# Performance work log

Measured on AMD Instinct MI355X. Metric: run time of the kernel, lower is better.

## Reference

```python
import jax, jax.numpy as jnp
import numpy as np

K_V = 0.5
G_OFF = 0.001
G_ON = 0.005
N_IN = 4096
N_OUT = 4096
BATCH = 8192


def setup_inputs() -> dict:
    key = jax.random.key(0)
    k1, k2, k3 = jax.random.split(key, 3)
    x = jax.random.normal(k1, (BATCH, N_IN), dtype=jnp.float32)
    # RandomNormal(stddev=1/sqrt(neurons_in)) initializer
    w = jax.random.normal(k2, (N_IN, N_OUT), dtype=jnp.float32) / np.sqrt(N_IN)
    # bias initialized to 0 in the module; use small noise so it is non-degenerate
    b = jax.random.normal(k3, (N_OUT,), dtype=jnp.float32) * 0.01
    return {"x": x, "w": w, "b": b}


def reference(x, w, b):
    # combine_weights: fold bias as an extra input row, x gets a ones column
    weights = jnp.concatenate([w, b[None, :]], axis=0)            # (n_in+1, n_out)
    ones = jnp.ones((x.shape[0], 1), dtype=x.dtype)
    voltages = K_V * jnp.concatenate([x, ones], axis=1)           # (B, n_in+1)

    # weights_to_conductances, 'lowest' mapping rule (differential pair)
    max_weight = jnp.max(jnp.abs(weights))
    k_cond = (G_ON - G_OFF) / max_weight
    g_eff = k_cond * weights
    g_pos = G_OFF + jnp.maximum(g_eff, 0.0)                       # even columns
    g_neg = G_OFF - jnp.minimum(g_eff, 0.0)                       # odd columns
    # interleave pos/neg -> (n_in+1, 2*n_out)
    conductances = jnp.stack([g_pos, g_neg], axis=-1).reshape(weights.shape[0], -1)

    # crossbar currents: scaled GEMM
    currents = voltages @ conductances                            # (B, 2*n_out)

    # differential current subtraction + rescale back to weight domain
    total_currents = currents[:, 0::2] - currents[:, 1::2]        # (B, n_out)
    y_disturbed = total_currents / (K_V * k_cond)
    return y_disturbed
```

## Files before the change

### kernel.cpp

```cpp
#include <hip/hip_runtime.h>
#include <cstdint>

typedef unsigned short u16;
typedef __attribute__((ext_vector_type(8))) __bf16 bf16x8;
typedef __attribute__((ext_vector_type(4))) float f32x4;

#define M_DIM 8192
#define N_DIM 4096
#define K_DIM 4096

#define CVT_X_BLOCKS 16384
#define CVT_W_BLOCKS 4096

__device__ __forceinline__ u16 f2bf(float f) {
    union { float f; uint32_t u; } v; v.f = f;
    uint32_t u = v.u;
    u += 0x7FFFu + ((u >> 16) & 1u);
    return (u16)(u >> 16);
}

__global__ __launch_bounds__(256) void cvt_kernel(const float* __restrict__ x,
                                                  const float* __restrict__ w,
                                                  u16* __restrict__ xb,
                                                  u16* __restrict__ wt) {
    const int t = threadIdx.x;
    if (blockIdx.x < CVT_X_BLOCKS) {
        size_t i = ((size_t)blockIdx.x * 256 + t) * 8;
        const float4* p = (const float4*)(x + i);
        float4 v0 = p[0], v1 = p[1];
        uint32_t o0 = (uint32_t)f2bf(v0.x) | ((uint32_t)f2bf(v0.y) << 16);
        uint32_t o1 = (uint32_t)f2bf(v0.z) | ((uint32_t)f2bf(v0.w) << 16);
        uint32_t o2 = (uint32_t)f2bf(v1.x) | ((uint32_t)f2bf(v1.y) << 16);
        uint32_t o3 = (uint32_t)f2bf(v1.z) | ((uint32_t)f2bf(v1.w) << 16);
        uint4 o; o.x = o0; o.y = o1; o.z = o2; o.w = o3;
        *(uint4*)(xb + i) = o;
    } else {
        __shared__ u16 lds[64 * 68];
        const int bid = blockIdx.x - CVT_X_BLOCKS;
        const int k0 = (bid & 63) * 64;
        const int n0 = (bid >> 6) * 64;
#pragma unroll
        for (int i = 0; i < 4; ++i) {
            int idx = i * 256 + t;
            int r = idx >> 4;
            int c4 = (idx & 15) * 4;
            float4 v = *(const float4*)&w[(size_t)(k0 + r) * N_DIM + n0 + c4];
            uint2 o;
            o.x = (uint32_t)f2bf(v.x) | ((uint32_t)f2bf(v.y) << 16);
            o.y = (uint32_t)f2bf(v.z) | ((uint32_t)f2bf(v.w) << 16);
            *(uint2*)&lds[r * 68 + c4] = o;
        }
        __syncthreads();
#pragma unroll
        for (int i = 0; i < 4; ++i) {
            int idx = i * 256 + t;
            int rn  = idx >> 4;
            int ck  = (idx & 15) * 4;
            uint2 o;
            o.x = (uint32_t)lds[(ck + 0) * 68 + rn] | ((uint32_t)lds[(ck + 1) * 68 + rn] << 16);
            o.y = (uint32_t)lds[(ck + 2) * 68 + rn] | ((uint32_t)lds[(ck + 3) * 68 + rn] << 16);
            *(uint2*)&wt[(size_t)(n0 + rn) * K_DIM + k0 + ck] = o;
        }
    }
}

typedef const uint32_t __attribute__((address_space(1)))* gp_t;
typedef uint32_t __attribute__((address_space(3)))* lp_t;

#define BK 64
#define NTILES (K_DIM / BK)
#define TN_TILES (N_DIM / 256)
#define NWG ((M_DIM / 256) * TN_TILES)

__global__ __launch_bounds__(512, 2) void gemm_kernel(const u16* __restrict__ A,
                                                      const u16* __restrict__ Bt,
                                                      const float* __restrict__ bias,
                                                      float* __restrict__ C) {
    __shared__ u16 As[2][2][256][32];
    __shared__ u16 Bs[2][2][256][32];

    const int t    = threadIdx.x;
    const int lane = t & 63;
    const int l16  = lane & 15;
    const int quad = lane >> 4;
    const int wave = t >> 6;
    const int wr   = wave >> 2;
    const int wc   = wave & 3;

    const int bid = blockIdx.x;
    const int wg  = (bid & 7) * (NWG >> 3) + (bid >> 3);
    const int bm  = (wg / TN_TILES) * 256;
    const int bn  = (wg % TN_TILES) * 256;

    const int rC0 = t >> 2;
    const int rC1 = rC0 + 128;
    const int kcS = ((t & 3) ^ ((rC0 >> 1) & 3)) * 8;
    const u16* a0 = A  + (size_t)(bm + rC0) * K_DIM + kcS;
    const u16* a1 = A  + (size_t)(bm + rC1) * K_DIM + kcS;
    const u16* b0 = Bt + (size_t)(bn + rC0) * K_DIM + kcS;
    const u16* b1 = Bt + (size_t)(bn + rC1) * K_DIM + kcS;

    const int sw8 = (quad ^ ((l16 >> 1) & 3)) * 8;

    f32x4 acc[8][4] = {};
    bf16x8 af[4], bf[4];

#define STAGE_A(buf, kh, kk) do {                                                                   \
        __builtin_amdgcn_global_load_lds((gp_t)(a0 + (kk) + (kh) * 32), (lp_t)&As[buf][kh][rC0][(t & 3) * 8], 16, 0, 0); \
        __builtin_amdgcn_global_load_lds((gp_t)(a1 + (kk) + (kh) * 32), (lp_t)&As[buf][kh][rC1][(t & 3) * 8], 16, 0, 0); \
    } while (0)
#define STAGE_B(buf, kh, kk) do {                                                                   \
        __builtin_amdgcn_global_load_lds((gp_t)(b0 + (kk) + (kh) * 32), (lp_t)&Bs[buf][kh][rC0][(t & 3) * 8], 16, 0, 0); \
        __builtin_amdgcn_global_load_lds((gp_t)(b1 + (kk) + (kh) * 32), (lp_t)&Bs[buf][kh][rC1][(t & 3) * 8], 16, 0, 0); \
    } while (0)
#define LDA(buf, kh, mbase)                                                                \
    _Pragma("unroll")                                                                      \
    for (int i = 0; i < 4; ++i)                                                            \
        af[i] = *(const bf16x8*)&As[buf][kh][wr * 128 + ((mbase) + i) * 16 + l16][sw8]
#define LDB(buf, kh)                                                                       \
    _Pragma("unroll")                                                                      \
    for (int j = 0; j < 4; ++j)                                                            \
        bf[j] = *(const bf16x8*)&Bs[buf][kh][wc * 64 + j * 16 + l16][sw8]
#define MFMA16(mbase)                                                                      \
    __builtin_amdgcn_s_setprio(1);                                                         \
    _Pragma("unroll")                                                                      \
    for (int i = 0; i < 4; ++i)                                                            \
        _Pragma("unroll")                                                                  \
        for (int j = 0; j < 4; ++j)                                                        \
            acc[(mbase) + i][j] =                                                          \
                __builtin_amdgcn_mfma_f32_16x16x32_bf16(af[i], bf[j], acc[(mbase) + i][j], 0, 0, 0); \
    __builtin_amdgcn_s_setprio(0)
#define FENCE() asm volatile("" ::: "memory")

    STAGE_A(0, 0, 0); STAGE_B(0, 0, 0);
    STAGE_A(0, 1, 0); STAGE_B(0, 1, 0);
    asm volatile("s_waitcnt vmcnt(4)" ::: "memory");
    __builtin_amdgcn_s_barrier();
    FENCE();

#pragma unroll 2
    for (int tt = 0; tt < NTILES; ++tt) {
        const int nb = tt & 1;
        const int pb = nb ^ 1;
        const int kn = (tt + 1 < NTILES) ? (tt + 1) * BK : 0;

        STAGE_A(pb, 0, kn);
        LDB(nb, 0);
        LDA(nb, 0, 0);
        MFMA16(0);
        STAGE_B(pb, 0, kn);
        LDA(nb, 0, 4);
        MFMA16(4);

        asm volatile("s_waitcnt vmcnt(4)" ::: "memory");
        __builtin_amdgcn_s_barrier();
        FENCE();

        STAGE_A(pb, 1, kn);
        LDB(nb, 1);
        LDA(nb, 1, 0);
        MFMA16(0);
        STAGE_B(pb, 1, kn);
        LDA(nb, 1, 4);
        MFMA16(4);

        asm volatile("s_waitcnt vmcnt(4)" ::: "memory");
        __builtin_amdgcn_s_barrier();
        FENCE();
    }

#pragma unroll
    for (int j = 0; j < 4; ++j) {
        const int col = bn + wc * 64 + j * 16 + l16;
        const float bv = bias[col];
#pragma unroll
        for (int i = 0; i < 8; ++i) {
            const int row = bm + wr * 128 + i * 16 + quad * 4;
#pragma unroll
            for (int r = 0; r < 4; ++r)
                C[(size_t)(row + r) * N_DIM + col] = acc[i][j][r] + bv;
        }
    }
#undef STAGE_A
#undef STAGE_B
#undef LDA
#undef LDB
#undef MFMA16
#undef FENCE
}

extern "C" void kernel_launch(void* const* d_in, const int* in_sizes, int n_in,
                              void* d_out, int out_size, void* d_ws, size_t ws_size,
                              hipStream_t stream) {
    const float* x = (const float*)d_in[0];
    const float* w = (const float*)d_in[1];
    const float* b = (const float*)d_in[2];
    float* out = (float*)d_out;

    u16* xb = (u16*)d_ws;
    u16* wt = xb + (size_t)M_DIM * K_DIM;

    cvt_kernel<<<CVT_X_BLOCKS + CVT_W_BLOCKS, 256, 0, stream>>>(x, w, xb, wt);
    gemm_kernel<<<dim3(NWG), 512, 0, stream>>>(xb, wt, b, out);
}
```

Measured before the change: 538.4 us.

## Transpose W in registers without LDS and simplify GEMM to BK=32 double buffering

The weight conversion kernel now transposes an 8x4 block per thread in registers and writes 16-byte rows of the transposed bf16 matrix, with no LDS staging and no block barrier. This halves the number of conversion blocks. The GEMM main loop drops the split-half K schedule, which interleaved staging, LDS reads and MFMAs. It now uses a plain K-tile of 32: issue the next tile's async loads, wait, barrier, load all fragments, run 32 MFMAs, then barrier again. This doubles the barriers per unit of K and removes the fine-grained overlap of loads with MFMA, so latency hiding may suffer.

New measurement: 553.8 us. +2.9%, slower.

```diff
diff --git a/kernel.cpp b/kernel.cpp
--- a/kernel.cpp
+++ b/kernel.cpp
@@ -10,7 +10,7 @@
 #define K_DIM 4096
 
 #define CVT_X_BLOCKS 16384
-#define CVT_W_BLOCKS 4096
+#define CVT_W_BLOCKS 2048
 
 __device__ __forceinline__ u16 f2bf(float f) {
     union { float f; uint32_t u; } v; v.f = f;
@@ -35,31 +35,30 @@
         uint4 o; o.x = o0; o.y = o1; o.z = o2; o.w = o3;
         *(uint4*)(xb + i) = o;
     } else {
-        __shared__ u16 lds[64 * 68];
         const int bid = blockIdx.x - CVT_X_BLOCKS;
         const int k0 = (bid & 63) * 64;
-        const int n0 = (bid >> 6) * 64;
+        const int n0 = (bid >> 6) * 128;
+        const int wv = t >> 6, l = t & 63;
+        const int a  = l & 7;
+        const int g  = l >> 3;
+        const int kk = k0 + a * 8;
+        const int nn = n0 + wv * 32 + g * 4;
+
+        uint32_t b[8][4];
+#pragma unroll
+        for (int j = 0; j < 8; ++j) {
+            float4 v = *(const float4*)&w[(size_t)(kk + j) * N_DIM + nn];
+            b[j][0] = f2bf(v.x); b[j][1] = f2bf(v.y);
+            b[j][2] = f2bf(v.z); b[j][3] = f2bf(v.w);
+        }
 #pragma unroll
         for (int i = 0; i < 4; ++i) {
-            int idx = i * 256 + t;
-            int r = idx >> 4;
-            int c4 = (idx & 15) * 4;
-            float4 v = *(const float4*)&w[(size_t)(k0 + r) * N_DIM + n0 + c4];
-            uint2 o;
-            o.x = (uint32_t)f2bf(v.x) | ((uint32_t)f2bf(v.y) << 16);
-            o.y = (uint32_t)f2bf(v.z) | ((uint32_t)f2bf(v.w) << 16);
-            *(uint2*)&lds[r * 68 + c4] = o;
-        }
-        __syncthreads();
-#pragma unroll
-        for (int i = 0; i < 4; ++i) {
-            int idx = i * 256 + t;
-            int rn  = idx >> 4;
-            int ck  = (idx & 15) * 4;
-            uint2 o;
-            o.x = (uint32_t)lds[(ck + 0) * 68 + rn] | ((uint32_t)lds[(ck + 1) * 68 + rn] << 16);
-            o.y = (uint32_t)lds[(ck + 2) * 68 + rn] | ((uint32_t)lds[(ck + 3) * 68 + rn] << 16);
-            *(uint2*)&wt[(size_t)(n0 + rn) * K_DIM + k0 + ck] = o;
+            uint4 o;
+            o.x = b[0][i] | (b[1][i] << 16);
+            o.y = b[2][i] | (b[3][i] << 16);
+            o.z = b[4][i] | (b[5][i] << 16);
+            o.w = b[6][i] | (b[7][i] << 16);
+            *(uint4*)&wt[(size_t)(nn + i) * K_DIM + kk] = o;
         }
     }
 }
@@ -67,7 +66,7 @@
 typedef const uint32_t __attribute__((address_space(1)))* gp_t;
 typedef uint32_t __attribute__((address_space(3)))* lp_t;
 
-#define BK 64
+#define BK 32
 #define NTILES (K_DIM / BK)
 #define TN_TILES (N_DIM / 256)
 #define NWG ((M_DIM / 256) * TN_TILES)
@@ -76,8 +75,8 @@
                                                       const u16* __restrict__ Bt,
                                                       const float* __restrict__ bias,
                                                       float* __restrict__ C) {
-    __shared__ u16 As[2][2][256][32];
-    __shared__ u16 Bs[2][2][256][32];
+    __shared__ u16 As[2][256][32];
+    __shared__ u16 Bs[2][256][32];
 
     const int t    = threadIdx.x;
     const int lane = t & 63;
@@ -103,40 +102,18 @@
     const int sw8 = (quad ^ ((l16 >> 1) & 3)) * 8;
 
     f32x4 acc[8][4] = {};
-    bf16x8 af[4], bf[4];
+    bf16x8 af[8], bf[4];
 
-#define STAGE_A(buf, kh, kk) do {                                                                   \
-        __builtin_amdgcn_global_load_lds((gp_t)(a0 + (kk) + (kh) * 32), (lp_t)&As[buf][kh][rC0][(t & 3) * 8], 16, 0, 0); \
-        __builtin_amdgcn_global_load_lds((gp_t)(a1 + (kk) + (kh) * 32), (lp_t)&As[buf][kh][rC1][(t & 3) * 8], 16, 0, 0); \
+#define STAGE_A(buf, kk) do {                                                                   \
+        __builtin_amdgcn_global_load_lds((gp_t)(a0 + (kk)), (lp_t)&As[buf][rC0][(t & 3) * 8], 16, 0, 0); \
+        __builtin_amdgcn_global_load_lds((gp_t)(a1 + (kk)), (lp_t)&As[buf][rC1][(t & 3) * 8], 16, 0, 0); \
     } while (0)
-#define STAGE_B(buf, kh, kk) do {                                                                   \
-        __builtin_amdgcn_global_load_lds((gp_t)(b0 + (kk) + (kh) * 32), (lp_t)&Bs[buf][kh][rC0][(t & 3) * 8], 16, 0, 0); \
-        __builtin_amdgcn_global_load_lds((gp_t)(b1 + (kk) + (kh) * 32), (lp_t)&Bs[buf][kh][rC1][(t & 3) * 8], 16, 0, 0); \
+#define STAGE_B(buf, kk) do {                                                                   \
+        __builtin_amdgcn_global_load_lds((gp_t)(b0 + (kk)), (lp_t)&Bs[buf][rC0][(t & 3) * 8], 16, 0, 0); \
+        __builtin_amdgcn_global_load_lds((gp_t)(b1 + (kk)), (lp_t)&Bs[buf][rC1][(t & 3) * 8], 16, 0, 0); \
     } while (0)
-#define LDA(buf, kh, mbase)                                                                \
-    _Pragma("unroll")                                                                      \
-    for (int i = 0; i < 4; ++i)                                                            \
-        af[i] = *(const bf16x8*)&As[buf][kh][wr * 128 + ((mbase) + i) * 16 + l16][sw8]
-#define LDB(buf, kh)                                                                       \
-    _Pragma("unroll")                                                                      \
-    for (int j = 0; j < 4; ++j)                                                            \
-        bf[j] = *(const bf16x8*)&Bs[buf][kh][wc * 64 + j * 16 + l16][sw8]
-#define MFMA16(mbase)                                                                      \
-    __builtin_amdgcn_s_setprio(1);                                                         \
-    _Pragma("unroll")                                                                      \
-    for (int i = 0; i < 4; ++i)                                                            \
-        _Pragma("unroll")                                                                  \
-        for (int j = 0; j < 4; ++j)                                                        \
-            acc[(mbase) + i][j] =                                                          \
-                __builtin_amdgcn_mfma_f32_16x16x32_bf16(af[i], bf[j], acc[(mbase) + i][j], 0, 0, 0); \
-    __builtin_amdgcn_s_setprio(0)
-#define FENCE() asm volatile("" ::: "memory")
 
-    STAGE_A(0, 0, 0); STAGE_B(0, 0, 0);
-    STAGE_A(0, 1, 0); STAGE_B(0, 1, 0);
-    asm volatile("s_waitcnt vmcnt(4)" ::: "memory");
-    __builtin_amdgcn_s_barrier();
-    FENCE();
+    STAGE_A(0, 0); STAGE_B(0, 0);
 
 #pragma unroll 2
     for (int tt = 0; tt < NTILES; ++tt) {
@@ -144,29 +121,26 @@
         const int pb = nb ^ 1;
         const int kn = (tt + 1 < NTILES) ? (tt + 1) * BK : 0;
 
-        STAGE_A(pb, 0, kn);
-        LDB(nb, 0);
-        LDA(nb, 0, 0);
-        MFMA16(0);
-        STAGE_B(pb, 0, kn);
-        LDA(nb, 0, 4);
-        MFMA16(4);
-
+        STAGE_A(pb, kn); STAGE_B(pb, kn);
         asm volatile("s_waitcnt vmcnt(4)" ::: "memory");
         __builtin_amdgcn_s_barrier();
-        FENCE();
 
-        STAGE_A(pb, 1, kn);
-        LDB(nb, 1);
-        LDA(nb, 1, 0);
-        MFMA16(0);
-        STAGE_B(pb, 1, kn);
-        LDA(nb, 1, 4);
-        MFMA16(4);
+#pragma unroll
+        for (int i = 0; i < 8; ++i)
+            af[i] = *(const bf16x8*)&As[nb][wr * 128 + i * 16 + l16][sw8];
+#pragma unroll
+        for (int j = 0; j < 4; ++j)
+            bf[j] = *(const bf16x8*)&Bs[nb][wc * 64 + j * 16 + l16][sw8];
 
-        asm volatile("s_waitcnt vmcnt(4)" ::: "memory");
+        __builtin_amdgcn_s_setprio(1);
+#pragma unroll
+        for (int i = 0; i < 8; ++i)
+#pragma unroll
+            for (int j = 0; j < 4; ++j)
+                acc[i][j] = __builtin_amdgcn_mfma_f32_16x16x32_bf16(af[i], bf[j], acc[i][j], 0, 0, 0);
+        __builtin_amdgcn_s_setprio(0);
+
         __builtin_amdgcn_s_barrier();
-        FENCE();
     }
 
 #pragma unroll
@@ -183,10 +157,6 @@
     }
 #undef STAGE_A
 #undef STAGE_B
-#undef LDA
-#undef LDB
-#undef MFMA16
-#undef FENCE
 }
 
 extern "C" void kernel_launch(void* const* d_in, const int* in_sizes, int n_in,
```
